# Optimization experiments

Measured on AMD Instinct MI355X. Metric: run time of the kernel, lower is better.

The kernel has to match this reference:

```python
import jax, jax.numpy as jnp
import numpy as np

PRED_LEN = 12
A = 128          # agents in the single scene
NHEAD = 8
NLAYERS = 2
D = 256          # embedding_dim
MLP = 1024
HDIM = 128       # decoder_h_dim
OBS_LEN = 8
MEMLEN = A * OBS_LEN
NEG = -1e9       # stands in for float('-inf') in the AR mask


def _sinusoid(length, d):
    pos = jnp.arange(length, dtype=jnp.float32)[:, None]
    div = jnp.exp(jnp.arange(0, d, 2, dtype=jnp.float32) * (-np.log(10000.0) / d))
    ang = pos * div
    pe = jnp.zeros((length, d), jnp.float32)
    pe = pe.at[:, 0::2].set(jnp.sin(ang))
    pe = pe.at[:, 1::2].set(jnp.cos(ang))
    return pe


def _ln(x, g, b):
    m = x.mean(-1, keepdims=True)
    v = ((x - m) ** 2).mean(-1, keepdims=True)
    return (x - m) / jnp.sqrt(v + 1e-5) * g + b


def _mha(q, k, v, Wq, bq, Wk, bk, Wv, bv, Wo, bo, mask):
    dh = D // NHEAD
    qh = (q @ Wq.T + bq).reshape(-1, NHEAD, dh)
    kh = (k @ Wk.T + bk).reshape(-1, NHEAD, dh)
    vh = (v @ Wv.T + bv).reshape(-1, NHEAD, dh)
    s = jnp.einsum('ihd,jhd->hij', qh, kh) / np.sqrt(dh) + mask[None]
    w = jax.nn.softmax(s, axis=-1)
    o = jnp.einsum('hij,jhd->ihd', w, vh).reshape(-1, D)
    return o @ Wo.T + bo


def _forward(last_pos, decoder_state, memory, agent_mask, in_W, in_b, out_W, out_b,
             sa_Wq, sa_bq, sa_Wk, sa_bk, sa_Wv, sa_bv, sa_Wo, sa_bo,
             ca_Wq, ca_bq, ca_Wk, ca_bk, ca_Wv, ca_bv, ca_Wo, ca_bo,
             ff_W1, ff_b1, ff_W2, ff_b2,
             ln1_g, ln1_b, ln2_g, ln2_b, ln3_g, ln3_b):
    agent_pe = _sinusoid(A, D)
    scene_pos = last_pos
    tokens = []
    outs = []
    for s in range(PRED_LEN):  # fixed-length AR loop (unrolled, static shapes)
        feat = jnp.concatenate([scene_pos, decoder_state], axis=-1)  # [A, 2+HDIM]
        tokens.append(feat @ in_W.T + in_b)                          # [A, D]
        steps = s + 1
        tgt = jnp.concatenate(tokens, axis=0)                        # [steps*A, D]
        time_enc = jnp.repeat(_sinusoid(steps, D), A, axis=0)
        x = tgt + time_enc + jnp.tile(agent_pe, (steps, 1))
        times = jnp.repeat(jnp.arange(steps), A)
        # generate_ar_mask: block-causal over time, tiled agent_mask within block
        tgt_mask = jnp.where(times[None, :] > times[:, None], NEG,
                             jnp.tile(agent_mask, (steps, steps)))
        # generate_mask: tiled agent_mask for cross-attention to memory
        mem_mask = jnp.tile(agent_mask, (steps, MEMLEN // A))
        for l in range(NLAYERS):
            sa = _mha(x, x, x, sa_Wq[l], sa_bq[l], sa_Wk[l], sa_bk[l],
                      sa_Wv[l], sa_bv[l], sa_Wo[l], sa_bo[l], tgt_mask)
            x = _ln(x + sa, ln1_g[l], ln1_b[l])
            ca = _mha(x, memory, memory, ca_Wq[l], ca_bq[l], ca_Wk[l], ca_bk[l],
                      ca_Wv[l], ca_bv[l], ca_Wo[l], ca_bo[l], mem_mask)
            x = _ln(x + ca, ln2_g[l], ln2_b[l])
            ff = jax.nn.relu(x @ ff_W1[l].T + ff_b1[l]) @ ff_W2[l].T + ff_b2[l]
            x = _ln(x + ff, ln3_g[l], ln3_b[l])
        rel = x[-A:] @ out_W.T + out_b                               # [A, 2]
        outs.append(rel)
        scene_pos = scene_pos + rel
    return jnp.stack(outs, axis=0)                                   # [PRED_LEN, A, 2]


def setup_inputs():
    key = jax.random.key(0)
    ks = jax.random.split(key, 40)
    def rn(k, shape, scale=0.02):
        return jax.random.normal(k, shape, jnp.float32) * scale
    inp = {
        'last_pos': jax.random.normal(ks[0], (A, 2), jnp.float32),
        'decoder_state': jax.random.normal(ks[1], (A, HDIM), jnp.float32),
        'memory': jax.random.normal(ks[2], (MEMLEN, D), jnp.float32),
        'agent_mask': jnp.zeros((A, A), jnp.float32),
        'in_W': rn(ks[3], (D, 2 + HDIM)),
        'in_b': jnp.zeros((D,), jnp.float32),
        'out_W': rn(ks[4], (2, D)),
        'out_b': jnp.zeros((2,), jnp.float32),
    }
    names = ['sa_Wq', 'sa_Wk', 'sa_Wv', 'sa_Wo', 'ca_Wq', 'ca_Wk', 'ca_Wv', 'ca_Wo']
    for i, n in enumerate(names):
        inp[n] = rn(ks[5 + i], (NLAYERS, D, D))
        inp[n.replace('W', 'b')] = jnp.zeros((NLAYERS, D), jnp.float32)
    inp['ff_W1'] = rn(ks[20], (NLAYERS, MLP, D))
    inp['ff_b1'] = jnp.zeros((NLAYERS, MLP), jnp.float32)
    inp['ff_W2'] = rn(ks[21], (NLAYERS, D, MLP))
    inp['ff_b2'] = jnp.zeros((NLAYERS, D), jnp.float32)
    for n in ['ln1', 'ln2', 'ln3']:
        inp[n + '_g'] = jnp.ones((NLAYERS, D), jnp.float32)
        inp[n + '_b'] = jnp.zeros((NLAYERS, D), jnp.float32)
    return inp


def reference(last_pos, decoder_state, memory, agent_mask, in_W, in_b, out_W, out_b,
              sa_Wq, sa_bq, sa_Wk, sa_bk, sa_Wv, sa_bv, sa_Wo, sa_bo,
              ca_Wq, ca_bq, ca_Wk, ca_bk, ca_Wv, ca_bv, ca_Wo, ca_bo,
              ff_W1, ff_b1, ff_W2, ff_b2,
              ln1_g, ln1_b, ln2_g, ln2_b, ln3_g, ln3_b):
    return _forward(last_pos, decoder_state, memory, agent_mask, in_W, in_b, out_W, out_b,
                    sa_Wq, sa_bq, sa_Wk, sa_bk, sa_Wv, sa_bv, sa_Wo, sa_bo,
                    ca_Wq, ca_bq, ca_Wk, ca_bk, ca_Wv, ca_bv, ca_Wo, ca_bo,
                    ff_W1, ff_b1, ff_W2, ff_b2,
                    ln1_g, ln1_b, ln2_g, ln2_b, ln3_g, ln3_b)
```

## Files before the change

### kernel.cpp

```cpp
#include <hip/hip_runtime.h>
#include <math.h>

#define AGENTS 128
#define DIM 256
#define NHEADS 8
#define MEM_LEN 1024
#define MLP_DIM 1024
#define PRED 12
#define MAXS (PRED * AGENTS)

typedef __attribute__((ext_vector_type(8))) short short8;
typedef __attribute__((ext_vector_type(4))) float f32x4;

#define MFMA(a, b, c) __builtin_amdgcn_mfma_f32_16x16x32_bf16(a, b, c, 0, 0, 0)

__device__ __forceinline__ unsigned short f2bf(float f) {
  union { float f; unsigned u; } v; v.f = f;
  unsigned r = v.u + 0x7fffu + ((v.u >> 16) & 1u);
  return (unsigned short)(r >> 16);
}

__device__ __forceinline__ short8 afrag8(const float* p) {
  float4 a = *(const float4*)p;
  float4 b = *(const float4*)(p + 4);
  short8 r;
  r[0] = (short)f2bf(a.x); r[1] = (short)f2bf(a.y);
  r[2] = (short)f2bf(a.z); r[3] = (short)f2bf(a.w);
  r[4] = (short)f2bf(b.x); r[5] = (short)f2bf(b.y);
  r[6] = (short)f2bf(b.z); r[7] = (short)f2bf(b.w);
  return r;
}

__device__ __forceinline__ void ln_stats(const float* __restrict__ pst, int row,
                                         float& mean, float& rstd) {
  float4 p0 = *(const float4*)(pst + row * 8);
  float4 p1 = *(const float4*)(pst + row * 8 + 4);
  float s  = p0.x + p0.z + p1.x + p1.z;
  float ss = p0.y + p0.w + p1.y + p1.w;
  mean = s * (1.0f / 256.0f);
  rstd = rsqrtf(ss * (1.0f / 256.0f) - mean * mean + 1e-5f);
}

__device__ __forceinline__ short8 afragLN(const float* __restrict__ yr,
                                          const float* __restrict__ lg,
                                          const float* __restrict__ lb,
                                          int k, float mean, float rstd) {
  float4 a = *(const float4*)(yr + k), b = *(const float4*)(yr + k + 4);
  float4 ga = *(const float4*)(lg + k), gb = *(const float4*)(lg + k + 4);
  float4 ba = *(const float4*)(lb + k), bb = *(const float4*)(lb + k + 4);
  short8 r;
  r[0] = (short)f2bf((a.x - mean) * rstd * ga.x + ba.x);
  r[1] = (short)f2bf((a.y - mean) * rstd * ga.y + ba.y);
  r[2] = (short)f2bf((a.z - mean) * rstd * ga.z + ba.z);
  r[3] = (short)f2bf((a.w - mean) * rstd * ga.w + ba.w);
  r[4] = (short)f2bf((b.x - mean) * rstd * gb.x + bb.x);
  r[5] = (short)f2bf((b.y - mean) * rstd * gb.y + bb.y);
  r[6] = (short)f2bf((b.z - mean) * rstd * gb.z + bb.z);
  r[7] = (short)f2bf((b.w - mean) * rstd * gb.w + bb.w);
  return r;
}

template <int AMODE, int RES, int EPI>
__global__ __launch_bounds__(256) void wproj_k(
    const unsigned short* __restrict__ ab, int lda,
    const float* __restrict__ Ya, const float* __restrict__ psta,
    const float* __restrict__ lga, const float* __restrict__ lba,
    const unsigned short* __restrict__ W, const float* __restrict__ bias, int K,
    const float* __restrict__ res,
    const float* __restrict__ Yp, const float* __restrict__ pstp,
    const float* __restrict__ gp, const float* __restrict__ bp,
    float* __restrict__ Yo, float* __restrict__ psto,
    unsigned short* __restrict__ mido)
{
  const int tid = threadIdx.x, l = tid & 63, w = tid >> 6;
  const int c15 = l & 15, g8 = (l >> 4) * 8, r0v = (l >> 4) * 4;
  const int rowb = blockIdx.x * 64 + w * 16;
  const int arow = rowb + c15;
  const int cb = blockIdx.y;
  const int colb = cb * 64;

  float meanA = 0.f, rstdA = 0.f;
  if (AMODE == 1) ln_stats(psta, arow, meanA, rstdA);

  const int KC = K >> 5;
  f32x4 acc[4] = {};
  const unsigned short* wp = W + (colb + c15) * K + g8;
  for (int kc = 0; kc < KC; ++kc) {
    short8 af;
    if (AMODE == 0) af = *(const short8*)(ab + arow * lda + kc * 32 + g8);
    else af = afragLN(Ya + arow * 256, lga, lba, kc * 32 + g8, meanA, rstdA);
#pragma unroll
    for (int t = 0; t < 4; ++t)
      acc[t] = MFMA(af, *(const short8*)(wp + t * 16 * K + kc * 32), acc[t]);
  }

  float mp[4], rp[4];
  if (RES == 2) {
#pragma unroll
    for (int r = 0; r < 4; ++r) ln_stats(pstp, rowb + r0v + r, mp[r], rp[r]);
  }

  float v[4][4];
#pragma unroll
  for (int t = 0; t < 4; ++t) {
    const int col = colb + t * 16 + c15;
    const float bb = bias[col];
    float gpp = 0.f, bpp = 0.f;
    if (RES == 2) { gpp = gp[col]; bpp = bp[col]; }
#pragma unroll
    for (int r = 0; r < 4; ++r) {
      const int row = rowb + r0v + r;
      float x = acc[t][r] + bb;
      if (RES == 1) x += res[row * 256 + col];
      if (RES == 2) x += (Yp[row * 256 + col] - mp[r]) * rp[r] * gpp + bpp;
      if (EPI == 0) Yo[row * 256 + col] = x;
      if (EPI == 1) mido[row * 1024 + col] = f2bf(fmaxf(x, 0.f));
      v[t][r] = x;
    }
  }
  if (EPI == 0) {
#pragma unroll
    for (int r = 0; r < 4; ++r) {
      float s  = v[0][r] + v[1][r] + v[2][r] + v[3][r];
      float ss = v[0][r]*v[0][r] + v[1][r]*v[1][r] + v[2][r]*v[2][r] + v[3][r]*v[3][r];
#pragma unroll
      for (int m = 1; m < 16; m <<= 1) {
        s  += __shfl_xor(s, m, 64);
        ss += __shfl_xor(ss, m, 64);
      }
      if (c15 == 0) {
        const int row = rowb + r0v + r;
        psto[row * 8 + cb * 2]     = s;
        psto[row * 8 + cb * 2 + 1] = ss;
      }
    }
  }
}

template <int AMODE>
__global__ __launch_bounds__(256) void kvproj_k(
    const unsigned short* __restrict__ ab, int lda,
    const float* __restrict__ Ya, const float* __restrict__ psta,
    const float* __restrict__ lga, const float* __restrict__ lba,
    const float* __restrict__ af32,
    const unsigned short* __restrict__ Wk, const float* __restrict__ bk,
    const unsigned short* __restrict__ Wv, const float* __restrict__ bv,
    unsigned short* __restrict__ Ko, unsigned short* __restrict__ Vo,
    int Spad, int crow)
{
  const int tid = threadIdx.x, l = tid & 63, w = tid >> 6;
  const int c15 = l & 15, g8 = (l >> 4) * 8, r0v = (l >> 4) * 4;
  const int rowb = blockIdx.x * 64 + w * 16;
  const int arow = rowb + c15;
  const int y = blockIdx.y;
  const bool isK = y < 4;
  const int colb = (y & 3) * 64;
  const unsigned short* W = isK ? Wk : Wv;
  const float* bias = isK ? bk : bv;

  float meanA = 0.f, rstdA = 0.f;
  if (AMODE == 1) ln_stats(psta, arow, meanA, rstdA);

  f32x4 acc[4] = {};
  const unsigned short* wp = W + (colb + c15) * 256 + g8;
  for (int kc = 0; kc < 8; ++kc) {
    short8 af;
    if (AMODE == 0) af = *(const short8*)(ab + arow * lda + kc * 32 + g8);
    else if (AMODE == 1) af = afragLN(Ya + arow * 256, lga, lba, kc * 32 + g8, meanA, rstdA);
    else af = afrag8(af32 + arow * 256 + kc * 32 + g8);
#pragma unroll
    for (int t = 0; t < 4; ++t)
      acc[t] = MFMA(af, *(const short8*)(wp + t * 16 * 256 + kc * 32), acc[t]);
  }
#pragma unroll
  for (int t = 0; t < 4; ++t) {
    const int col = colb + t * 16 + c15;
    const float bb = bias[col];
    const int hh = col >> 5, d = col & 31;
#pragma unroll
    for (int r = 0; r < 4; ++r) {
      const int row = crow + rowb + r0v + r;
      unsigned short val = f2bf(acc[t][r] + bb);
      if (isK) Ko[hh * Spad * 32 + row * 32 + d] = val;
      else     Vo[col * Spad + row] = val;
    }
  }
}

template <int AMODE>
__global__ __launch_bounds__(256) void attn2_k(
    const unsigned short* __restrict__ ab,
    const float* __restrict__ Ya, const float* __restrict__ psta,
    const float* __restrict__ lga, const float* __restrict__ lba,
    const unsigned short* __restrict__ Wq, const float* __restrict__ bq,
    const unsigned short* __restrict__ Kc, const unsigned short* __restrict__ Vt,
    const float* __restrict__ mask, unsigned short* __restrict__ Ob,
    int S, int Spad)
{
  __shared__ unsigned short sq[4][16][32];
  __shared__ unsigned short ps[4][16][96];
  const int tid = threadIdx.x, l = tid & 63, w = tid >> 6;
  const int c15 = l & 15, g = l >> 4, g8 = g * 8, r0v = g * 4;
  const int h = blockIdx.y;
  const int rowb = blockIdx.x * 64 + w * 16;
  const int arow = rowb + c15;

  float meanA = 0.f, rstdA = 0.f;
  if (AMODE == 1) ln_stats(psta, arow, meanA, rstdA);
  f32x4 q0 = {}, q1 = {};
  const unsigned short* wp = Wq + (h * 32 + c15) * 256 + g8;
  for (int kc = 0; kc < 8; ++kc) {
    short8 af;
    if (AMODE == 0) af = *(const short8*)(ab + arow * 256 + kc * 32 + g8);
    else af = afragLN(Ya + arow * 256, lga, lba, kc * 32 + g8, meanA, rstdA);
    q0 = MFMA(af, *(const short8*)(wp + kc * 32), q0);
    q1 = MFMA(af, *(const short8*)(wp + 16 * 256 + kc * 32), q1);
  }
  {
    const float b0 = bq[h * 32 + c15], b1 = bq[h * 32 + 16 + c15];
#pragma unroll
    for (int r = 0; r < 4; ++r) {
      sq[w][r0v + r][c15]      = f2bf(q0[r] + b0);
      sq[w][r0v + r][16 + c15] = f2bf(q1[r] + b1);
    }
  }
  short8 qf = *(const short8*)&sq[w][c15][g8];

  float mk[2][4][4];
#pragma unroll
  for (int p = 0; p < 2; ++p)
#pragma unroll
    for (int t = 0; t < 4; ++t)
#pragma unroll
      for (int r = 0; r < 4; ++r)
        mk[p][t][r] = mask[arow * AGENTS + p * 64 + t * 16 + g * 4 + r];

  const unsigned short* kh = Kc + h * Spad * 32;
  const unsigned short* vh = Vt + h * 32 * Spad;
  unsigned short* pq = &ps[w][0][0];
  const float scale = 0.17677669529663687f;
  f32x4 oa0 = {}, oa1 = {};
  float lsum = 0.f;

  for (int kc = 0; kc < S; kc += 64) {
    const int p = (kc >> 6) & 1;
#pragma unroll
    for (int t = 0; t < 4; ++t) {
      short8 kf = *(const short8*)(kh + (kc + t * 16 + c15) * 32 + g8);
      f32x4 zz = {};
      f32x4 sc = MFMA(kf, qf, zz);
      float e0 = __expf(sc[0] * scale + mk[p][t][0]);
      float e1 = __expf(sc[1] * scale + mk[p][t][1]);
      float e2 = __expf(sc[2] * scale + mk[p][t][2]);
      float e3 = __expf(sc[3] * scale + mk[p][t][3]);
      unsigned short b0 = f2bf(e0), b1 = f2bf(e1), b2 = f2bf(e2), b3 = f2bf(e3);
      union { unsigned u; float f; } c0, c1, c2, c3;
      c0.u = (unsigned)b0 << 16; c1.u = (unsigned)b1 << 16;
      c2.u = (unsigned)b2 << 16; c3.u = (unsigned)b3 << 16;
      lsum += c0.f + c1.f + c2.f + c3.f;
      uint2 u2;
      u2.x = (unsigned)b0 | ((unsigned)b1 << 16);
      u2.y = (unsigned)b2 | ((unsigned)b3 << 16);
      *(uint2*)&pq[c15 * 96 + t * 16 + g * 4] = u2;
    }
#pragma unroll
    for (int ks = 0; ks < 2; ++ks) {
      short8 pf = *(const short8*)&pq[c15 * 96 + ks * 32 + g8];
      short8 v0 = *(const short8*)(vh + c15 * Spad + kc + ks * 32 + g8);
      short8 v1 = *(const short8*)(vh + (16 + c15) * Spad + kc + ks * 32 + g8);
      oa0 = MFMA(v0, pf, oa0);
      oa1 = MFMA(v1, pf, oa1);
    }
  }
  lsum += __shfl_xor(lsum, 16, 64);
  lsum += __shfl_xor(lsum, 32, 64);
  const float inv = 1.0f / lsum;
#pragma unroll
  for (int r = 0; r < 4; ++r) {
    Ob[arow * DIM + h * 32 + g * 4 + r]      = f2bf(oa0[r] * inv);
    Ob[arow * DIM + h * 32 + 16 + g * 4 + r] = f2bf(oa1[r] * inv);
  }
}

__global__ __launch_bounds__(256) void embed_k(
    const float* __restrict__ scene, const float* __restrict__ ds,
    const unsigned short* __restrict__ inWb, const float* __restrict__ inb,
    const float* __restrict__ peA, const float* __restrict__ peT,
    float* __restrict__ x0, unsigned short* __restrict__ xb0, int step)
{
  const int tid = threadIdx.x, l = tid & 63, w = tid >> 6;
  const int c15 = l & 15, g8 = (l >> 4) * 8, r0v = (l >> 4) * 4;
  const int rowb = blockIdx.x * 64 + w * 16;
  const int arow = rowb + c15;
  const int colb = blockIdx.y * 64;
  f32x4 acc[4] = {};
  const unsigned short* wp = inWb + (colb + c15) * 160 + g8;
  for (int kc = 0; kc < 5; ++kc) {
    short8 af;
#pragma unroll
    for (int j = 0; j < 8; ++j) {
      int kk = kc * 32 + g8 + j;
      float v = (kk < 2) ? scene[arow * 2 + kk]
                         : ((kk < 130) ? ds[arow * 128 + (kk - 2)] : 0.f);
      af[j] = (short)f2bf(v);
    }
#pragma unroll
    for (int t = 0; t < 4; ++t)
      acc[t] = MFMA(af, *(const short8*)(wp + t * 16 * 160 + kc * 32), acc[t]);
  }
#pragma unroll
  for (int t = 0; t < 4; ++t) {
    const int col = colb + t * 16 + c15;
    const float bb = inb[col] + peT[step * DIM + col];
#pragma unroll
    for (int r = 0; r < 4; ++r) {
      const int row = rowb + r0v + r;
      float v = acc[t][r] + bb + peA[row * DIM + col];
      x0[row * DIM + col] = v;
      xb0[row * DIM + col] = f2bf(v);
    }
  }
}

__global__ __launch_bounds__(256) void outp_k(
    const float* __restrict__ Y3, const float* __restrict__ pst3,
    const float* __restrict__ g3, const float* __restrict__ b3,
    const float* __restrict__ outW, const float* __restrict__ outB,
    float* __restrict__ outbuf, float* __restrict__ scene, int step)
{
  const int tid = threadIdx.x;
  const int row = tid >> 1, j = tid & 1;
  float mean, rstd;
  ln_stats(pst3, row, mean, rstd);
  const float* yr = Y3 + row * 256;
  const float* wr = outW + j * 256;
  float a = 0.f;
  for (int k = 0; k < 256; k += 4) {
    float4 y = *(const float4*)(yr + k);
    float4 gg = *(const float4*)(g3 + k);
    float4 bb = *(const float4*)(b3 + k);
    float4 ww = *(const float4*)(wr + k);
    a += ((y.x - mean) * rstd * gg.x + bb.x) * ww.x
       + ((y.y - mean) * rstd * gg.y + bb.y) * ww.y
       + ((y.z - mean) * rstd * gg.z + bb.z) * ww.z
       + ((y.w - mean) * rstd * gg.w + bb.w) * ww.w;
  }
  a += outB[j];
  outbuf[(step * AGENTS + row) * 2 + j] = a;
  scene[row * 2 + j] += a;
}

__global__ void cvt8_k(const float* p0, const float* p1, const float* p2,
                       const float* p3, const float* p4, const float* p5,
                       const float* p6, const float* p7, unsigned short* dst)
{
  const float* s;
  switch (blockIdx.z) {
    case 0: s = p0; break; case 1: s = p1; break;
    case 2: s = p2; break; case 3: s = p3; break;
    case 4: s = p4; break; case 5: s = p5; break;
    case 6: s = p6; break; default: s = p7; break;
  }
  int i = blockIdx.x * 256 + threadIdx.x;
  dst[blockIdx.z * 131072 + i] = f2bf(s[i]);
}

__global__ void cvtff_k(const float* w1, const float* w2, unsigned short* dst)
{
  const float* s = blockIdx.z ? w2 : w1;
  int i = blockIdx.x * 256 + threadIdx.x;
  dst[blockIdx.z * 524288 + i] = f2bf(s[i]);
}

__global__ void cvtinw_k(const float* w, unsigned short* dst)
{
  int i = blockIdx.x * 256 + threadIdx.x;
  if (i >= 256 * 160) return;
  int n = i / 160, k = i - n * 160;
  dst[i] = (k < 130) ? f2bf(w[n * 130 + k]) : (unsigned short)0;
}

__global__ void pe_k(float* peA, float* peT)
{
  int i = blockIdx.x * 256 + threadIdx.x;
  if (i < 128 * 256) {
    int row = i >> 8, c = i & 255, p = c >> 1;
    float dv = expf((float)(2 * p) * (-9.210340371976184f / 256.f));
    float ang = (float)row * dv;
    peA[i] = (c & 1) ? cosf(ang) : sinf(ang);
  } else if (i < 140 * 256) {
    int j = i - 32768;
    int s = j >> 8, c = j & 255, p = c >> 1;
    float dv = expf((float)(2 * p) * (-9.210340371976184f / 256.f));
    float ang = (float)s * dv;
    peT[j] = (c & 1) ? cosf(ang) : sinf(ang);
  }
}

extern "C" void kernel_launch(void* const* d_in, const int* in_sizes, int n_in,
                              void* d_out, int out_size, void* d_ws, size_t ws_size,
                              hipStream_t stream)
{
  const float* last_pos      = (const float*)d_in[0];
  const float* decoder_state = (const float*)d_in[1];
  const float* memory        = (const float*)d_in[2];
  const float* agent_mask    = (const float*)d_in[3];
  const float* in_W  = (const float*)d_in[4];
  const float* in_b  = (const float*)d_in[5];
  const float* out_W = (const float*)d_in[6];
  const float* out_b = (const float*)d_in[7];
  const float* sa_bq = (const float*)d_in[9];
  const float* sa_bk = (const float*)d_in[11];
  const float* sa_bv = (const float*)d_in[13];
  const float* sa_bo = (const float*)d_in[15];
  const float* ca_bq = (const float*)d_in[17];
  const float* ca_bk = (const float*)d_in[19];
  const float* ca_bv = (const float*)d_in[21];
  const float* ca_bo = (const float*)d_in[23];
  const float* ff_W1 = (const float*)d_in[24];
  const float* ff_b1 = (const float*)d_in[25];
  const float* ff_W2 = (const float*)d_in[26];
  const float* ff_b2 = (const float*)d_in[27];
  const float* ln1_g = (const float*)d_in[28];
  const float* ln1_b = (const float*)d_in[29];
  const float* ln2_g = (const float*)d_in[30];
  const float* ln2_b = (const float*)d_in[31];
  const float* ln3_g = (const float*)d_in[32];
  const float* ln3_b = (const float*)d_in[33];
  float* out = (float*)d_out;

  float* ws    = (float*)d_ws;
  float* scene = ws;
  float* x0    = scene + 256;
  float* Y1    = x0 + 32768;
  float* Y2    = Y1 + 32768;
  float* Y3    = Y2 + 32768;
  float* pst1  = Y3 + 32768;
  float* pst2  = pst1 + 1024;
  float* pst3  = pst2 + 1024;
  float* peA   = pst3 + 1024;
  float* peT   = peA + 32768;
  unsigned short* xb0   = (unsigned short*)(peT + 3072);
  unsigned short* abuf  = xb0 + 32768;
  unsigned short* mid   = abuf + 32768;
  unsigned short* saK   = mid + 131072;
  unsigned short* saV   = saK + 2 * MAXS * 256;
  unsigned short* memK  = saV + 2 * MAXS * 256;
  unsigned short* memV  = memK + 2 * MEM_LEN * 256;
  unsigned short* dxdb  = memV + 2 * MEM_LEN * 256;
  unsigned short* ffW1b = dxdb + 8 * 131072;
  unsigned short* ffW2b = ffW1b + 524288;
  unsigned short* inWb  = ffW2b + 524288;

  const dim3 blk(256);

  cvt8_k<<<dim3(512, 1, 8), blk, 0, stream>>>(
      (const float*)d_in[8], (const float*)d_in[10], (const float*)d_in[12],
      (const float*)d_in[14], (const float*)d_in[16], (const float*)d_in[18],
      (const float*)d_in[20], (const float*)d_in[22], dxdb);
  cvtff_k<<<dim3(2048, 1, 2), blk, 0, stream>>>(ff_W1, ff_W2, ffW1b);
  cvtinw_k<<<160, blk, 0, stream>>>(in_W, inWb);
  pe_k<<<140, blk, 0, stream>>>(peA, peT);
  for (int l = 0; l < 2; ++l) {
    kvproj_k<2><<<dim3(16, 8), blk, 0, stream>>>(
        nullptr, 0, nullptr, nullptr, nullptr, nullptr, memory,
        dxdb + 5 * 131072 + l * 65536, ca_bk + l * 256,
        dxdb + 6 * 131072 + l * 65536, ca_bv + l * 256,
        memK + l * 262144, memV + l * 262144, MEM_LEN, 0);
  }
  hipMemcpyAsync(scene, last_pos, 256 * sizeof(float), hipMemcpyDeviceToDevice, stream);

  for (int s = 0; s < PRED; ++s) {
    embed_k<<<dim3(2, 4), blk, 0, stream>>>(scene, decoder_state, inWb, in_b,
                                            peA, peT, x0, xb0, s);
    for (int l = 0; l < 2; ++l) {
      const unsigned short* saWq = dxdb + 0 * 131072 + l * 65536;
      const unsigned short* saWk = dxdb + 1 * 131072 + l * 65536;
      const unsigned short* saWv = dxdb + 2 * 131072 + l * 65536;
      const unsigned short* saWo = dxdb + 3 * 131072 + l * 65536;
      const unsigned short* caWq = dxdb + 4 * 131072 + l * 65536;
      const unsigned short* caWo = dxdb + 7 * 131072 + l * 65536;
      unsigned short* saKl = saK + l * MAXS * 256;
      unsigned short* saVl = saV + l * MAXS * 256;
      unsigned short* memKl = memK + l * 262144;
      unsigned short* memVl = memV + l * 262144;

      if (l == 0) {
        kvproj_k<0><<<dim3(2, 8), blk, 0, stream>>>(
            xb0, 256, nullptr, nullptr, nullptr, nullptr, nullptr,
            saWk, sa_bk, saWv, sa_bv, saKl, saVl, MAXS, s * AGENTS);
        attn2_k<0><<<dim3(2, 8), blk, 0, stream>>>(
            xb0, nullptr, nullptr, nullptr, nullptr,
            saWq, sa_bq, saKl, saVl, agent_mask, abuf, (s + 1) * AGENTS, MAXS);
        wproj_k<0, 1, 0><<<dim3(2, 4), blk, 0, stream>>>(
            abuf, 256, nullptr, nullptr, nullptr, nullptr,
            saWo, sa_bo, 256, x0, nullptr, nullptr, nullptr, nullptr,
            Y1, pst1, nullptr);
      } else {
        kvproj_k<1><<<dim3(2, 8), blk, 0, stream>>>(
            nullptr, 0, Y3, pst3, ln3_g, ln3_b, nullptr,
            saWk, sa_bk + 256, saWv, sa_bv + 256, saKl, saVl, MAXS, s * AGENTS);
        attn2_k<1><<<dim3(2, 8), blk, 0, stream>>>(
            nullptr, Y3, pst3, ln3_g, ln3_b,
            saWq, sa_bq + 256, saKl, saVl, agent_mask, abuf, (s + 1) * AGENTS, MAXS);
        wproj_k<0, 2, 0><<<dim3(2, 4), blk, 0, stream>>>(
            abuf, 256, nullptr, nullptr, nullptr, nullptr,
            saWo, sa_bo + 256, 256, nullptr, Y3, pst3, ln3_g, ln3_b,
            Y1, pst1, nullptr);
      }
      attn2_k<1><<<dim3(2, 8), blk, 0, stream>>>(
          nullptr, Y1, pst1, ln1_g + l * 256, ln1_b + l * 256,
          caWq, ca_bq + l * 256, memKl, memVl, agent_mask, abuf, MEM_LEN, MEM_LEN);
      wproj_k<0, 2, 0><<<dim3(2, 4), blk, 0, stream>>>(
          abuf, 256, nullptr, nullptr, nullptr, nullptr,
          caWo, ca_bo + l * 256, 256, nullptr, Y1, pst1, ln1_g + l * 256, ln1_b + l * 256,
          Y2, pst2, nullptr);
      wproj_k<1, 0, 1><<<dim3(2, 16), blk, 0, stream>>>(
          nullptr, 0, Y2, pst2, ln2_g + l * 256, ln2_b + l * 256,
          ffW1b + l * 262144, ff_b1 + l * 1024, 256,
          nullptr, nullptr, nullptr, nullptr, nullptr,
          nullptr, nullptr, mid);
      wproj_k<0, 2, 0><<<dim3(2, 4), blk, 0, stream>>>(
          mid, 1024, nullptr, nullptr, nullptr, nullptr,
          ffW2b + l * 262144, ff_b2 + l * 256, 1024,
          nullptr, Y2, pst2, ln2_g + l * 256, ln2_b + l * 256,
          Y3, pst3, nullptr);
    }
    outp_k<<<1, blk, 0, stream>>>(Y3, pst3, ln3_g + 256, ln3_b + 256,
                                  out_W, out_b, out, scene, s);
  }
}
```

Before: 2.481 ms.

## Fuse self-attention KV projection into attention and output head into embed

Self-attention K/V projection is folded into the attention kernel: each block recomputes K/V for all 128 new-step rows of its head, keeping them in LDS for the fresh keys, and writes its own 64-row half to global. The output projection and scene update are merged into the next step's embedding kernel, with a per-step scene array replacing in-place updates and one trailing launch emitting the final output. This removes two launches per layer per step plus the output launch, cutting launch and dependency overhead in a latency-bound AR loop. The cost is duplicated K/V projection work across the two row blocks and a redundant output-head computation in each embed block.

```diff
diff --git a/kernel.cpp b/kernel.cpp
--- a/kernel.cpp
+++ b/kernel.cpp
@@ -19,7 +19,9 @@
   unsigned r = v.u + 0x7fffu + ((v.u >> 16) & 1u);
   return (unsigned short)(r >> 16);
 }
-
+__device__ __forceinline__ float bfval(unsigned short b) {
+  union { unsigned u; float f; } v; v.u = (unsigned)b << 16; return v.f;
+}
 __device__ __forceinline__ short8 afrag8(const float* p) {
   float4 a = *(const float4*)p;
   float4 b = *(const float4*)(p + 4);
@@ -60,6 +62,309 @@
   return r;
 }
 
+__device__ __forceinline__ void score_tile(short8 kf, short8 qf, const float* m4,
+                                           unsigned short* dst, float& lsum) {
+  const float scale = 0.17677669529663687f;
+  f32x4 zz = {};
+  f32x4 sc = MFMA(kf, qf, zz);
+  unsigned short b0 = f2bf(__expf(sc[0] * scale + m4[0]));
+  unsigned short b1 = f2bf(__expf(sc[1] * scale + m4[1]));
+  unsigned short b2 = f2bf(__expf(sc[2] * scale + m4[2]));
+  unsigned short b3 = f2bf(__expf(sc[3] * scale + m4[3]));
+  lsum += bfval(b0) + bfval(b1) + bfval(b2) + bfval(b3);
+  uint2 u2;
+  u2.x = (unsigned)b0 | ((unsigned)b1 << 16);
+  u2.y = (unsigned)b2 | ((unsigned)b3 << 16);
+  *(uint2*)dst = u2;
+}
+
+__global__ __launch_bounds__(256) void embed2_k(
+    const float* __restrict__ last_pos, const float* __restrict__ ds,
+    const unsigned short* __restrict__ inWb, const float* __restrict__ inb,
+    const float* __restrict__ peA, const float* __restrict__ peT,
+    const float* __restrict__ Y3, const float* __restrict__ pst3,
+    const float* __restrict__ g3, const float* __restrict__ b3,
+    const float* __restrict__ outW, const float* __restrict__ outB,
+    float* __restrict__ out, float* __restrict__ sceneArr,
+    float* __restrict__ x0, unsigned short* __restrict__ xb0, int s)
+{
+  __shared__ float sscene[64][2];
+  const int rb = blockIdx.x, cb = blockIdx.y;
+  const int tid = threadIdx.x;
+  if (tid < 128) {
+    const int lrow = tid >> 1, j = tid & 1;
+    const int row = rb * 64 + lrow;
+    float sv;
+    if (s > 0) {
+      float mean, rstd; ln_stats(pst3, row, mean, rstd);
+      const float* yr = Y3 + row * 256;
+      const float* wr = outW + j * 256;
+      float a = 0.f;
+      for (int k = 0; k < 256; k += 4) {
+        float4 y = *(const float4*)(yr + k);
+        float4 gg = *(const float4*)(g3 + k);
+        float4 bb = *(const float4*)(b3 + k);
+        float4 ww = *(const float4*)(wr + k);
+        a += ((y.x - mean) * rstd * gg.x + bb.x) * ww.x
+           + ((y.y - mean) * rstd * gg.y + bb.y) * ww.y
+           + ((y.z - mean) * rstd * gg.z + bb.z) * ww.z
+           + ((y.w - mean) * rstd * gg.w + bb.w) * ww.w;
+      }
+      a += outB[j];
+      if (cb == 0) out[((s - 1) * AGENTS + row) * 2 + j] = a;
+      sv = sceneArr[(s - 1) * 256 + row * 2 + j] + a;
+    } else {
+      sv = last_pos[row * 2 + j];
+    }
+    if (s < PRED) {
+      sceneArr[s * 256 + row * 2 + j] = sv;
+      sscene[lrow][j] = sv;
+    }
+  }
+  __syncthreads();
+  if (s == PRED) return;
+
+  const int l = tid & 63, w = tid >> 6;
+  const int c15 = l & 15, g8 = (l >> 4) * 8, r0v = (l >> 4) * 4;
+  const int rowb = rb * 64 + w * 16;
+  const int arow = rowb + c15;
+  const int lsrow = w * 16 + c15;
+  const int colb = cb * 64;
+  f32x4 acc[4] = {};
+  const unsigned short* wp = inWb + (colb + c15) * 160 + g8;
+  for (int kc = 0; kc < 5; ++kc) {
+    short8 af;
+#pragma unroll
+    for (int j = 0; j < 8; ++j) {
+      int kk = kc * 32 + g8 + j;
+      float v = (kk < 2) ? sscene[lsrow][kk]
+                         : ((kk < 130) ? ds[arow * 128 + (kk - 2)] : 0.f);
+      af[j] = (short)f2bf(v);
+    }
+#pragma unroll
+    for (int t = 0; t < 4; ++t)
+      acc[t] = MFMA(af, *(const short8*)(wp + t * 16 * 160 + kc * 32), acc[t]);
+  }
+#pragma unroll
+  for (int t = 0; t < 4; ++t) {
+    const int col = colb + t * 16 + c15;
+    const float bb = inb[col] + peT[s * DIM + col];
+#pragma unroll
+    for (int r = 0; r < 4; ++r) {
+      const int row = rowb + r0v + r;
+      float v = acc[t][r] + bb + peA[row * DIM + col];
+      x0[row * DIM + col] = v;
+      xb0[row * DIM + col] = f2bf(v);
+    }
+  }
+}
+
+template <int AMODE>
+__global__ __launch_bounds__(256) void attnsa_k(
+    const unsigned short* __restrict__ ab,
+    const float* __restrict__ Ya, const float* __restrict__ psta,
+    const float* __restrict__ lga, const float* __restrict__ lba,
+    const unsigned short* __restrict__ Wq, const float* __restrict__ bq,
+    const unsigned short* __restrict__ Wk, const float* __restrict__ bk,
+    const unsigned short* __restrict__ Wv, const float* __restrict__ bv,
+    unsigned short* __restrict__ Ko, unsigned short* __restrict__ Vo,
+    const float* __restrict__ mask, unsigned short* __restrict__ Ob, int s)
+{
+  __shared__ unsigned short klds[128][32];
+  __shared__ unsigned short vlds[32][128];
+  __shared__ unsigned short sq[4][16][32];
+  __shared__ unsigned short ps[4][16][96];
+  const int rb = blockIdx.x, h = blockIdx.y;
+  const int tid = threadIdx.x, l = tid & 63, w = tid >> 6;
+  const int c15 = l & 15, g = l >> 4, g8 = g * 8, r0v = g * 4;
+
+#pragma unroll
+  for (int ti = 0; ti < 2; ++ti) {
+    const int arow = w * 32 + ti * 16 + c15;
+    float mean = 0.f, rstd = 0.f;
+    if (AMODE == 1) ln_stats(psta, arow, mean, rstd);
+    short8 af[8];
+#pragma unroll
+    for (int kc = 0; kc < 8; ++kc)
+      af[kc] = (AMODE == 0) ? *(const short8*)(ab + arow * 256 + kc * 32 + g8)
+                            : afragLN(Ya + arow * 256, lga, lba, kc * 32 + g8,
+                                      mean, rstd);
+#pragma unroll
+    for (int ct = 0; ct < 2; ++ct) {
+      const int col = h * 32 + ct * 16 + c15;
+      const int lc = ct * 16 + c15;
+      f32x4 acck = {}, accv = {};
+      const unsigned short* wpk = Wk + col * 256 + g8;
+      const unsigned short* wpv = Wv + col * 256 + g8;
+#pragma unroll
+      for (int kc = 0; kc < 8; ++kc) {
+        acck = MFMA(af[kc], *(const short8*)(wpk + kc * 32), acck);
+        accv = MFMA(af[kc], *(const short8*)(wpv + kc * 32), accv);
+      }
+      const float bbk = bk[col], bbv = bv[col];
+#pragma unroll
+      for (int r = 0; r < 4; ++r) {
+        const int row = w * 32 + ti * 16 + r0v + r;
+        unsigned short kvv = f2bf(acck[r] + bbk);
+        unsigned short vvv = f2bf(accv[r] + bbv);
+        klds[row][lc] = kvv;
+        vlds[lc][row] = vvv;
+        if ((row >> 6) == rb) {
+          Ko[h * (MAXS * 32) + (s * 128 + row) * 32 + lc] = kvv;
+          Vo[col * MAXS + s * 128 + row] = vvv;
+        }
+      }
+    }
+  }
+
+  {
+    const int arow = rb * 64 + w * 16 + c15;
+    float mean = 0.f, rstd = 0.f;
+    if (AMODE == 1) ln_stats(psta, arow, mean, rstd);
+    f32x4 q0 = {}, q1 = {};
+    const unsigned short* wp0 = Wq + (h * 32 + c15) * 256 + g8;
+    const unsigned short* wp1 = Wq + (h * 32 + 16 + c15) * 256 + g8;
+    for (int kc = 0; kc < 8; ++kc) {
+      short8 af = (AMODE == 0) ? *(const short8*)(ab + arow * 256 + kc * 32 + g8)
+                               : afragLN(Ya + arow * 256, lga, lba,
+                                         kc * 32 + g8, mean, rstd);
+      q0 = MFMA(af, *(const short8*)(wp0 + kc * 32), q0);
+      q1 = MFMA(af, *(const short8*)(wp1 + kc * 32), q1);
+    }
+    const float b0 = bq[h * 32 + c15], b1 = bq[h * 32 + 16 + c15];
+#pragma unroll
+    for (int r = 0; r < 4; ++r) {
+      sq[w][r0v + r][c15]      = f2bf(q0[r] + b0);
+      sq[w][r0v + r][16 + c15] = f2bf(q1[r] + b1);
+    }
+  }
+  __syncthreads();
+  short8 qf = *(const short8*)&sq[w][c15][g8];
+
+  const int qrow = rb * 64 + w * 16 + c15;
+  float mk[2][4][4];
+#pragma unroll
+  for (int pp = 0; pp < 2; ++pp)
+#pragma unroll
+    for (int t = 0; t < 4; ++t)
+#pragma unroll
+      for (int r = 0; r < 4; ++r)
+        mk[pp][t][r] = mask[qrow * AGENTS + pp * 64 + t * 16 + g * 4 + r];
+
+  const unsigned short* kh = Ko + h * (MAXS * 32);
+  const unsigned short* vh = Vo + h * 32 * MAXS;
+  const int S = (s + 1) * 128, fb = S - 128;
+  f32x4 oa0 = {}, oa1 = {};
+  float lsum = 0.f;
+  unsigned short* psrow = &ps[w][c15][0];
+
+  for (int kc = 0; kc < S; kc += 64) {
+    const int pp = (kc >> 6) & 1;
+    const bool fresh = kc >= fb;
+#pragma unroll
+    for (int t = 0; t < 4; ++t) {
+      const int key = kc + t * 16 + c15;
+      short8 kf = fresh ? *(const short8*)&klds[key - fb][g8]
+                        : *(const short8*)(kh + key * 32 + g8);
+      score_tile(kf, qf, mk[pp][t], psrow + t * 16 + g * 4, lsum);
+    }
+#pragma unroll
+    for (int ks = 0; ks < 2; ++ks) {
+      short8 pf = *(const short8*)(psrow + ks * 32 + g8);
+      const int j = kc + ks * 32 + g8;
+      short8 v0 = fresh ? *(const short8*)&vlds[c15][j - fb]
+                        : *(const short8*)(vh + c15 * MAXS + j);
+      short8 v1 = fresh ? *(const short8*)&vlds[16 + c15][j - fb]
+                        : *(const short8*)(vh + (16 + c15) * MAXS + j);
+      oa0 = MFMA(v0, pf, oa0);
+      oa1 = MFMA(v1, pf, oa1);
+    }
+  }
+  lsum += __shfl_xor(lsum, 16, 64);
+  lsum += __shfl_xor(lsum, 32, 64);
+  const float inv = 1.0f / lsum;
+#pragma unroll
+  for (int r = 0; r < 4; ++r) {
+    Ob[qrow * DIM + h * 32 + g * 4 + r]      = f2bf(oa0[r] * inv);
+    Ob[qrow * DIM + h * 32 + 16 + g * 4 + r] = f2bf(oa1[r] * inv);
+  }
+}
+
+__global__ __launch_bounds__(256) void attnca_k(
+    const float* __restrict__ Ya, const float* __restrict__ psta,
+    const float* __restrict__ lga, const float* __restrict__ lba,
+    const unsigned short* __restrict__ Wq, const float* __restrict__ bq,
+    const unsigned short* __restrict__ Kc, const unsigned short* __restrict__ Vt,
+    const float* __restrict__ mask, unsigned short* __restrict__ Ob)
+{
+  __shared__ unsigned short sq[4][16][32];
+  __shared__ unsigned short ps[4][16][96];
+  const int rb = blockIdx.x, h = blockIdx.y;
+  const int tid = threadIdx.x, l = tid & 63, w = tid >> 6;
+  const int c15 = l & 15, g = l >> 4, g8 = g * 8, r0v = g * 4;
+  const int arow = rb * 64 + w * 16 + c15;
+
+  float mean, rstd;
+  ln_stats(psta, arow, mean, rstd);
+  f32x4 q0 = {}, q1 = {};
+  const unsigned short* wp = Wq + (h * 32 + c15) * 256 + g8;
+  for (int kc = 0; kc < 8; ++kc) {
+    short8 af = afragLN(Ya + arow * 256, lga, lba, kc * 32 + g8, mean, rstd);
+    q0 = MFMA(af, *(const short8*)(wp + kc * 32), q0);
+    q1 = MFMA(af, *(const short8*)(wp + 16 * 256 + kc * 32), q1);
+  }
+  {
+    const float b0 = bq[h * 32 + c15], b1 = bq[h * 32 + 16 + c15];
+#pragma unroll
+    for (int r = 0; r < 4; ++r) {
+      sq[w][r0v + r][c15]      = f2bf(q0[r] + b0);
+      sq[w][r0v + r][16 + c15] = f2bf(q1[r] + b1);
+    }
+  }
+  short8 qf = *(const short8*)&sq[w][c15][g8];
+
+  float mk[2][4][4];
+#pragma unroll
+  for (int pp = 0; pp < 2; ++pp)
+#pragma unroll
+    for (int t = 0; t < 4; ++t)
+#pragma unroll
+      for (int r = 0; r < 4; ++r)
+        mk[pp][t][r] = mask[arow * AGENTS + pp * 64 + t * 16 + g * 4 + r];
+
+  const unsigned short* kh = Kc + h * MEM_LEN * 32;
+  const unsigned short* vh = Vt + h * 32 * MEM_LEN;
+  unsigned short* psrow = &ps[w][c15][0];
+  f32x4 oa0 = {}, oa1 = {};
+  float lsum = 0.f;
+
+  for (int kc = 0; kc < MEM_LEN; kc += 64) {
+    const int pp = (kc >> 6) & 1;
+#pragma unroll
+    for (int t = 0; t < 4; ++t) {
+      short8 kf = *(const short8*)(kh + (kc + t * 16 + c15) * 32 + g8);
+      score_tile(kf, qf, mk[pp][t], psrow + t * 16 + g * 4, lsum);
+    }
+#pragma unroll
+    for (int ks = 0; ks < 2; ++ks) {
+      short8 pf = *(const short8*)(psrow + ks * 32 + g8);
+      const int j = kc + ks * 32 + g8;
+      short8 v0 = *(const short8*)(vh + c15 * MEM_LEN + j);
+      short8 v1 = *(const short8*)(vh + (16 + c15) * MEM_LEN + j);
+      oa0 = MFMA(v0, pf, oa0);
+      oa1 = MFMA(v1, pf, oa1);
+    }
+  }
+  lsum += __shfl_xor(lsum, 16, 64);
+  lsum += __shfl_xor(lsum, 32, 64);
+  const float inv = 1.0f / lsum;
+#pragma unroll
+  for (int r = 0; r < 4; ++r) {
+    Ob[arow * DIM + h * 32 + g * 4 + r]      = f2bf(oa0[r] * inv);
+    Ob[arow * DIM + h * 32 + 16 + g * 4 + r] = f2bf(oa1[r] * inv);
+  }
+}
+
 template <int AMODE, int RES, int EPI>
 __global__ __launch_bounds__(256) void wproj_k(
     const unsigned short* __restrict__ ab, int lda,
@@ -137,16 +442,11 @@
   }
 }
 
-template <int AMODE>
-__global__ __launch_bounds__(256) void kvproj_k(
-    const unsigned short* __restrict__ ab, int lda,
-    const float* __restrict__ Ya, const float* __restrict__ psta,
-    const float* __restrict__ lga, const float* __restrict__ lba,
-    const float* __restrict__ af32,
+__global__ __launch_bounds__(256) void memkv_k(
+    const float* __restrict__ mem,
     const unsigned short* __restrict__ Wk, const float* __restrict__ bk,
     const unsigned short* __restrict__ Wv, const float* __restrict__ bv,
-    unsigned short* __restrict__ Ko, unsigned short* __restrict__ Vo,
-    int Spad, int crow)
+    unsigned short* __restrict__ Ko, unsigned short* __restrict__ Vo)
 {
   const int tid = threadIdx.x, l = tid & 63, w = tid >> 6;
   const int c15 = l & 15, g8 = (l >> 4) * 8, r0v = (l >> 4) * 4;
@@ -158,16 +458,10 @@
   const unsigned short* W = isK ? Wk : Wv;
   const float* bias = isK ? bk : bv;
 
-  float meanA = 0.f, rstdA = 0.f;
-  if (AMODE == 1) ln_stats(psta, arow, meanA, rstdA);
-
   f32x4 acc[4] = {};
   const unsigned short* wp = W + (colb + c15) * 256 + g8;
   for (int kc = 0; kc < 8; ++kc) {
-    short8 af;
-    if (AMODE == 0) af = *(const short8*)(ab + arow * lda + kc * 32 + g8);
-    else if (AMODE == 1) af = afragLN(Ya + arow * 256, lga, lba, kc * 32 + g8, meanA, rstdA);
-    else af = afrag8(af32 + arow * 256 + kc * 32 + g8);
+    short8 af = afrag8(mem + arow * 256 + kc * 32 + g8);
 #pragma unroll
     for (int t = 0; t < 4; ++t)
       acc[t] = MFMA(af, *(const short8*)(wp + t * 16 * 256 + kc * 32), acc[t]);
@@ -179,175 +473,12 @@
     const int hh = col >> 5, d = col & 31;
 #pragma unroll
     for (int r = 0; r < 4; ++r) {
-      const int row = crow + rowb + r0v + r;
+      const int row = rowb + r0v + r;
       unsigned short val = f2bf(acc[t][r] + bb);
-      if (isK) Ko[hh * Spad * 32 + row * 32 + d] = val;
-      else     Vo[col * Spad + row] = val;
-    }
-  }
-}
-
-template <int AMODE>
-__global__ __launch_bounds__(256) void attn2_k(
-    const unsigned short* __restrict__ ab,
-    const float* __restrict__ Ya, const float* __restrict__ psta,
-    const float* __restrict__ lga, const float* __restrict__ lba,
-    const unsigned short* __restrict__ Wq, const float* __restrict__ bq,
-    const unsigned short* __restrict__ Kc, const unsigned short* __restrict__ Vt,
-    const float* __restrict__ mask, unsigned short* __restrict__ Ob,
-    int S, int Spad)
-{
-  __shared__ unsigned short sq[4][16][32];
-  __shared__ unsigned short ps[4][16][96];
-  const int tid = threadIdx.x, l = tid & 63, w = tid >> 6;
-  const int c15 = l & 15, g = l >> 4, g8 = g * 8, r0v = g * 4;
-  const int h = blockIdx.y;
-  const int rowb = blockIdx.x * 64 + w * 16;
-  const int arow = rowb + c15;
-
-  float meanA = 0.f, rstdA = 0.f;
-  if (AMODE == 1) ln_stats(psta, arow, meanA, rstdA);
-  f32x4 q0 = {}, q1 = {};
-  const unsigned short* wp = Wq + (h * 32 + c15) * 256 + g8;
-  for (int kc = 0; kc < 8; ++kc) {
-    short8 af;
-    if (AMODE == 0) af = *(const short8*)(ab + arow * 256 + kc * 32 + g8);
-    else af = afragLN(Ya + arow * 256, lga, lba, kc * 32 + g8, meanA, rstdA);
-    q0 = MFMA(af, *(const short8*)(wp + kc * 32), q0);
-    q1 = MFMA(af, *(const short8*)(wp + 16 * 256 + kc * 32), q1);
-  }
-  {
-    const float b0 = bq[h * 32 + c15], b1 = bq[h * 32 + 16 + c15];
-#pragma unroll
-    for (int r = 0; r < 4; ++r) {
-      sq[w][r0v + r][c15]      = f2bf(q0[r] + b0);
-      sq[w][r0v + r][16 + c15] = f2bf(q1[r] + b1);
-    }
-  }
-  short8 qf = *(const short8*)&sq[w][c15][g8];
-
-  float mk[2][4][4];
-#pragma unroll
-  for (int p = 0; p < 2; ++p)
-#pragma unroll
-    for (int t = 0; t < 4; ++t)
-#pragma unroll
-      for (int r = 0; r < 4; ++r)
-        mk[p][t][r] = mask[arow * AGENTS + p * 64 + t * 16 + g * 4 + r];
-
-  const unsigned short* kh = Kc + h * Spad * 32;
-  const unsigned short* vh = Vt + h * 32 * Spad;
-  unsigned short* pq = &ps[w][0][0];
-  const float scale = 0.17677669529663687f;
-  f32x4 oa0 = {}, oa1 = {};
-  float lsum = 0.f;
-
-  for (int kc = 0; kc < S; kc += 64) {
-    const int p = (kc >> 6) & 1;
-#pragma unroll
-    for (int t = 0; t < 4; ++t) {
-      short8 kf = *(const short8*)(kh + (kc + t * 16 + c15) * 32 + g8);
-      f32x4 zz = {};
-      f32x4 sc = MFMA(kf, qf, zz);
-      float e0 = __expf(sc[0] * scale + mk[p][t][0]);
-      float e1 = __expf(sc[1] * scale + mk[p][t][1]);
-      float e2 = __expf(sc[2] * scale + mk[p][t][2]);
-      float e3 = __expf(sc[3] * scale + mk[p][t][3]);
-      unsigned short b0 = f2bf(e0), b1 = f2bf(e1), b2 = f2bf(e2), b3 = f2bf(e3);
-      union { unsigned u; float f; } c0, c1, c2, c3;
-      c0.u = (unsigned)b0 << 16; c1.u = (unsigned)b1 << 16;
-      c2.u = (unsigned)b2 << 16; c3.u = (unsigned)b3 << 16;
-      lsum += c0.f + c1.f + c2.f + c3.f;
-      uint2 u2;
-      u2.x = (unsigned)b0 | ((unsigned)b1 << 16);
-      u2.y = (unsigned)b2 | ((unsigned)b3 << 16);
-      *(uint2*)&pq[c15 * 96 + t * 16 + g * 4] = u2;
-    }
-#pragma unroll
-    for (int ks = 0; ks < 2; ++ks) {
-      short8 pf = *(const short8*)&pq[c15 * 96 + ks * 32 + g8];
-      short8 v0 = *(const short8*)(vh + c15 * Spad + kc + ks * 32 + g8);
-      short8 v1 = *(const short8*)(vh + (16 + c15) * Spad + kc + ks * 32 + g8);
-      oa0 = MFMA(v0, pf, oa0);
-      oa1 = MFMA(v1, pf, oa1);
-    }
-  }
-  lsum += __shfl_xor(lsum, 16, 64);
-  lsum += __shfl_xor(lsum, 32, 64);
-  const float inv = 1.0f / lsum;
-#pragma unroll
-  for (int r = 0; r < 4; ++r) {
-    Ob[arow * DIM + h * 32 + g * 4 + r]      = f2bf(oa0[r] * inv);
-    Ob[arow * DIM + h * 32 + 16 + g * 4 + r] = f2bf(oa1[r] * inv);
-  }
-}
-
-__global__ __launch_bounds__(256) void embed_k(
-    const float* __restrict__ scene, const float* __restrict__ ds,
-    const unsigned short* __restrict__ inWb, const float* __restrict__ inb,
-    const float* __restrict__ peA, const float* __restrict__ peT,
-    float* __restrict__ x0, unsigned short* __restrict__ xb0, int step)
-{
-  const int tid = threadIdx.x, l = tid & 63, w = tid >> 6;
-  const int c15 = l & 15, g8 = (l >> 4) * 8, r0v = (l >> 4) * 4;
-  const int rowb = blockIdx.x * 64 + w * 16;
-  const int arow = rowb + c15;
-  const int colb = blockIdx.y * 64;
-  f32x4 acc[4] = {};
-  const unsigned short* wp = inWb + (colb + c15) * 160 + g8;
-  for (int kc = 0; kc < 5; ++kc) {
-    short8 af;
-#pragma unroll
-    for (int j = 0; j < 8; ++j) {
-      int kk = kc * 32 + g8 + j;
-      float v = (kk < 2) ? scene[arow * 2 + kk]
-                         : ((kk < 130) ? ds[arow * 128 + (kk - 2)] : 0.f);
-      af[j] = (short)f2bf(v);
-    }
-#pragma unroll
-    for (int t = 0; t < 4; ++t)
-      acc[t] = MFMA(af, *(const short8*)(wp + t * 16 * 160 + kc * 32), acc[t]);
-  }
-#pragma unroll
-  for (int t = 0; t < 4; ++t) {
-    const int col = colb + t * 16 + c15;
-    const float bb = inb[col] + peT[step * DIM + col];
-#pragma unroll
-    for (int r = 0; r < 4; ++r) {
-      const int row = rowb + r0v + r;
-      float v = acc[t][r] + bb + peA[row * DIM + col];
-      x0[row * DIM + col] = v;
-      xb0[row * DIM + col] = f2bf(v);
-    }
-  }
-}
-
-__global__ __launch_bounds__(256) void outp_k(
-    const float* __restrict__ Y3, const float* __restrict__ pst3,
-    const float* __restrict__ g3, const float* __restrict__ b3,
-    const float* __restrict__ outW, const float* __restrict__ outB,
-    float* __restrict__ outbuf, float* __restrict__ scene, int step)
-{
-  const int tid = threadIdx.x;
-  const int row = tid >> 1, j = tid & 1;
-  float mean, rstd;
-  ln_stats(pst3, row, mean, rstd);
-  const float* yr = Y3 + row * 256;
-  const float* wr = outW + j * 256;
-  float a = 0.f;
-  for (int k = 0; k < 256; k += 4) {
-    float4 y = *(const float4*)(yr + k);
-    float4 gg = *(const float4*)(g3 + k);
-    float4 bb = *(const float4*)(b3 + k);
-    float4 ww = *(const float4*)(wr + k);
-    a += ((y.x - mean) * rstd * gg.x + bb.x) * ww.x
-       + ((y.y - mean) * rstd * gg.y + bb.y) * ww.y
-       + ((y.z - mean) * rstd * gg.z + bb.z) * ww.z
-       + ((y.w - mean) * rstd * gg.w + bb.w) * ww.w;
-  }
-  a += outB[j];
-  outbuf[(step * AGENTS + row) * 2 + j] = a;
-  scene[row * 2 + j] += a;
+      if (isK) Ko[hh * MEM_LEN * 32 + row * 32 + d] = val;
+      else     Vo[col * MEM_LEN + row] = val;
+    }
+  }
 }
 
 __global__ void cvt8_k(const float* p0, const float* p1, const float* p2,
@@ -417,9 +548,7 @@
   const float* ca_bk = (const float*)d_in[19];
   const float* ca_bv = (const float*)d_in[21];
   const float* ca_bo = (const float*)d_in[23];
-  const float* ff_W1 = (const float*)d_in[24];
   const float* ff_b1 = (const float*)d_in[25];
-  const float* ff_W2 = (const float*)d_in[26];
   const float* ff_b2 = (const float*)d_in[27];
   const float* ln1_g = (const float*)d_in[28];
   const float* ln1_b = (const float*)d_in[29];
@@ -429,17 +558,17 @@
   const float* ln3_b = (const float*)d_in[33];
   float* out = (float*)d_out;
 
-  float* ws    = (float*)d_ws;
-  float* scene = ws;
-  float* x0    = scene + 256;
-  float* Y1    = x0 + 32768;
-  float* Y2    = Y1 + 32768;
-  float* Y3    = Y2 + 32768;
-  float* pst1  = Y3 + 32768;
-  float* pst2  = pst1 + 1024;
-  float* pst3  = pst2 + 1024;
-  float* peA   = pst3 + 1024;
-  float* peT   = peA + 32768;
+  float* ws       = (float*)d_ws;
+  float* sceneArr = ws;
+  float* x0       = sceneArr + 13 * 256;
+  float* Y1       = x0 + 32768;
+  float* Y2       = Y1 + 32768;
+  float* Y3       = Y2 + 32768;
+  float* pst1     = Y3 + 32768;
+  float* pst2     = pst1 + 1024;
+  float* pst3     = pst2 + 1024;
+  float* peA      = pst3 + 1024;
+  float* peT      = peA + 32768;
   unsigned short* xb0   = (unsigned short*)(peT + 3072);
   unsigned short* abuf  = xb0 + 32768;
   unsigned short* mid   = abuf + 32768;
@@ -458,21 +587,24 @@
       (const float*)d_in[8], (const float*)d_in[10], (const float*)d_in[12],
       (const float*)d_in[14], (const float*)d_in[16], (const float*)d_in[18],
       (const float*)d_in[20], (const float*)d_in[22], dxdb);
-  cvtff_k<<<dim3(2048, 1, 2), blk, 0, stream>>>(ff_W1, ff_W2, ffW1b);
+  cvtff_k<<<dim3(2048, 1, 2), blk, 0, stream>>>((const float*)d_in[24],
+                                                (const float*)d_in[26], ffW1b);
   cvtinw_k<<<160, blk, 0, stream>>>(in_W, inWb);
   pe_k<<<140, blk, 0, stream>>>(peA, peT);
   for (int l = 0; l < 2; ++l) {
-    kvproj_k<2><<<dim3(16, 8), blk, 0, stream>>>(
-        nullptr, 0, nullptr, nullptr, nullptr, nullptr, memory,
+    memkv_k<<<dim3(16, 8), blk, 0, stream>>>(
+        memory,
         dxdb + 5 * 131072 + l * 65536, ca_bk + l * 256,
         dxdb + 6 * 131072 + l * 65536, ca_bv + l * 256,
-        memK + l * 262144, memV + l * 262144, MEM_LEN, 0);
-  }
-  hipMemcpyAsync(scene, last_pos, 256 * sizeof(float), hipMemcpyDeviceToDevice, stream);
+        memK + l * MEM_LEN * 256, memV + l * MEM_LEN * 256);
+  }
 
   for (int s = 0; s < PRED; ++s) {
-    embed_k<<<dim3(2, 4), blk, 0, stream>>>(scene, decoder_state, inWb, in_b,
-                                            peA, peT, x0, xb0, s);
+    embed2_k<<<dim3(2, 4), blk, 0, stream>>>(
+        last_pos, decoder_state, inWb, in_b, peA, peT,
+        Y3, pst3, ln3_g + 256, ln3_b + 256, out_W, out_b,
+        out, sceneArr, x0, xb0, s);
+
     for (int l = 0; l < 2; ++l) {
       const unsigned short* saWq = dxdb + 0 * 131072 + l * 65536;
       const unsigned short* saWk = dxdb + 1 * 131072 + l * 65536;
@@ -482,38 +614,35 @@
       const unsigned short* caWo = dxdb + 7 * 131072 + l * 65536;
       unsigned short* saKl = saK + l * MAXS * 256;
       unsigned short* saVl = saV + l * MAXS * 256;
-      unsigned short* memKl = memK + l * 262144;
-      unsigned short* memVl = memV + l * 262144;
 
       if (l == 0) {
-        kvproj_k<0><<<dim3(2, 8), blk, 0, stream>>>(
-            xb0, 256, nullptr, nullptr, nullptr, nullptr, nullptr,
-            saWk, sa_bk, saWv, sa_bv, saKl, saVl, MAXS, s * AGENTS);
-        attn2_k<0><<<dim3(2, 8), blk, 0, stream>>>(
+        attnsa_k<0><<<dim3(2, 8), blk, 0, stream>>>(
             xb0, nullptr, nullptr, nullptr, nullptr,
-            saWq, sa_bq, saKl, saVl, agent_mask, abuf, (s + 1) * AGENTS, MAXS);
+            saWq, sa_bq, saWk, sa_bk, saWv, sa_bv,
+            saKl, saVl, agent_mask, abuf, s);
         wproj_k<0, 1, 0><<<dim3(2, 4), blk, 0, stream>>>(
             abuf, 256, nullptr, nullptr, nullptr, nullptr,
             saWo, sa_bo, 256, x0, nullptr, nullptr, nullptr, nullptr,
             Y1, pst1, nullptr);
       } else {
-        kvproj_k<1><<<dim3(2, 8), blk, 0, stream>>>(
-            nullptr, 0, Y3, pst3, ln3_g, ln3_b, nullptr,
-            saWk, sa_bk + 256, saWv, sa_bv + 256, saKl, saVl, MAXS, s * AGENTS);
-        attn2_k<1><<<dim3(2, 8), blk, 0, stream>>>(
+        attnsa_k<1><<<dim3(2, 8), blk, 0, stream>>>(
             nullptr, Y3, pst3, ln3_g, ln3_b,
-            saWq, sa_bq + 256, saKl, saVl, agent_mask, abuf, (s + 1) * AGENTS, MAXS);
+            saWq, sa_bq + 256, saWk, sa_bk + 256, saWv, sa_bv + 256,
+            saKl, saVl, agent_mask, abuf, s);
         wproj_k<0, 2, 0><<<dim3(2, 4), blk, 0, stream>>>(
             abuf, 256, nullptr, nullptr, nullptr, nullptr,
             saWo, sa_bo + 256, 256, nullptr, Y3, pst3, ln3_g, ln3_b,
             Y1, pst1, nullptr);
       }
-      attn2_k<1><<<dim3(2, 8), blk, 0, stream>>>(
-          nullptr, Y1, pst1, ln1_g + l * 256, ln1_b + l * 256,
-          caWq, ca_bq + l * 256, memKl, memVl, agent_mask, abuf, MEM_LEN, MEM_LEN);
+      attnca_k<<<dim3(2, 8), blk, 0, stream>>>(
+          Y1, pst1, ln1_g + l * 256, ln1_b + l * 256,
+          caWq, ca_bq + l * 256,
+          memK + l * MEM_LEN * 256, memV + l * MEM_LEN * 256,
+          agent_mask, abuf);
       wproj_k<0, 2, 0><<<dim3(2, 4), blk, 0, stream>>>(
           abuf, 256, nullptr, nullptr, nullptr, nullptr,
-          caWo, ca_bo + l * 256, 256, nullptr, Y1, pst1, ln1_g + l * 256, ln1_b + l * 256,
+          caWo, ca_bo + l * 256, 256, nullptr, Y1, pst1,
+          ln1_g + l * 256, ln1_b + l * 256,
           Y2, pst2, nullptr);
       wproj_k<1, 0, 1><<<dim3(2, 16), blk, 0, stream>>>(
           nullptr, 0, Y2, pst2, ln2_g + l * 256, ln2_b + l * 256,
@@ -526,7 +655,9 @@
           nullptr, Y2, pst2, ln2_g + l * 256, ln2_b + l * 256,
           Y3, pst3, nullptr);
     }
-    outp_k<<<1, blk, 0, stream>>>(Y3, pst3, ln3_g + 256, ln3_b + 256,
-                                  out_W, out_b, out, scene, s);
-  }
-}
+  }
+  embed2_k<<<dim3(2, 1), blk, 0, stream>>>(
+      last_pos, decoder_state, inWb, in_b, peA, peT,
+      Y3, pst3, ln3_g + 256, ln3_b + 256, out_W, out_b,
+      out, sceneArr, x0, xb0, PRED);
+}
```

Result: slower. 2.659 ms (+7.2%).
